# Optimization experiments

Measured on AMD Instinct MI355X. Metric: run time of the kernel, lower is better.

## Reference

```python
import jax, jax.numpy as jnp
import numpy as np

N_VOX = 500_000
C = 128
HID = 4 * C
RES = 128  # voxel grid resolution
K_OFFS = 27


def _build_sparse_coords_and_neighbors(seed=0):
    rng = np.random.default_rng(seed)
    lin = rng.choice(RES ** 3, size=N_VOX, replace=False)
    z = lin // (RES * RES)
    y = (lin // RES) % RES
    x = lin % RES
    # padded grid (RES+2)^3 so boundary lookups are in-bounds
    P = RES + 2
    grid = -np.ones(P * P * P, dtype=np.int64)
    z1, y1, x1 = z + 1, y + 1, x + 1
    grid[z1 * P * P + y1 * P + x1] = np.arange(N_VOX)
    offs = np.array([[dz, dy, dx] for dz in (-1, 0, 1) for dy in (-1, 0, 1) for dx in (-1, 0, 1)], dtype=np.int64)  # [27,3]
    nz = z1[:, None] + offs[None, :, 0]
    ny = y1[:, None] + offs[None, :, 1]
    nx = x1[:, None] + offs[None, :, 2]
    nbr = grid[nz * P * P + ny * P + nx]  # [N,27], -1 if neighbor voxel inactive
    return nbr.astype(np.int32)


def setup_inputs() -> dict:
    key = jax.random.key(0)
    ks = jax.random.split(key, 8)
    nbr = _build_sparse_coords_and_neighbors()
    scale = 0.02
    return {
        "feats": jax.random.normal(ks[0], (N_VOX, C), jnp.float32),
        "neighbor_idx": jnp.asarray(nbr),
        "conv_w": jax.random.normal(ks[1], (K_OFFS, C, C), jnp.float32) * scale,
        "conv_b": jax.random.normal(ks[2], (C,), jnp.float32) * scale,
        "ln_g": jnp.ones((C,), jnp.float32),
        "ln_b": jnp.zeros((C,), jnp.float32),
        "w1": jax.random.normal(ks[3], (C, HID), jnp.float32) * scale,
        "b1": jax.random.normal(ks[4], (HID,), jnp.float32) * scale,
        "w2": jax.random.normal(ks[5], (HID, C), jnp.float32) * scale,
        "b2": jax.random.normal(ks[6], (C,), jnp.float32) * scale,
    }


def _forward(feats, neighbor_idx, conv_w, conv_b, ln_g, ln_b, w1, b1, w2, b2):
    n, c = feats.shape
    # submanifold sparse conv3d: pad a zero row for missing (-1) neighbors
    f_pad = jnp.concatenate([feats, jnp.zeros((1, c), feats.dtype)], axis=0)
    idx = jnp.where(neighbor_idx < 0, n, neighbor_idx)  # [N,27]
    h = jnp.broadcast_to(conv_b, (n, c))
    for k in range(K_OFFS):  # fixed small kernel-offset loop; per-offset gather + GEMM
        h = h + f_pad[idx[:, k]] @ conv_w[k]
    # LayerNorm32 (fp32 math), eps=1e-6, affine
    h32 = h.astype(jnp.float32)
    mu = h32.mean(-1, keepdims=True)
    var = h32.var(-1, keepdims=True)
    hn = ((h32 - mu) * jax.lax.rsqrt(var + 1e-6) * ln_g + ln_b).astype(feats.dtype)
    # MLP: Linear -> SiLU -> Linear
    m = jax.nn.silu(hn @ w1 + b1) @ w2 + b2
    # residual h + x on sparse feats
    return m + feats


def reference(feats, neighbor_idx, conv_w, conv_b, ln_g, ln_b, w1, b1, w2, b2):
    return _forward(feats, neighbor_idx, conv_w, conv_b, ln_g, ln_b, w1, b1, w2, b2)
```

## Files before the change

kernel.cpp:

```cpp
#include <hip/hip_runtime.h>
#include <stdint.h>

#define NVOX 500000
#define NPAD 500224
#define ZERO_OFF (NVOX * 128)

typedef float  f32x4  __attribute__((ext_vector_type(4)));
typedef short  short8 __attribute__((ext_vector_type(8)));

__device__ __forceinline__ short f2bf(float x){
  unsigned u = __float_as_uint(x);
  unsigned r = (u + 0x7fffu + ((u >> 16) & 1u)) >> 16;
  return (short)r;
}

__device__ __forceinline__ void gload_lds16(const void* g, void* l){
  __builtin_amdgcn_global_load_lds(
      (const __attribute__((address_space(1))) unsigned int*)(uintptr_t)g,
      (__attribute__((address_space(3))) unsigned int*)(unsigned int)(uintptr_t)l,
      16, 0, 0);
}

__global__ void cast_feats_kernel(const float* __restrict__ f, short* __restrict__ t){
  long i = ((long)blockIdx.x * 256 + threadIdx.x) * 8;
  float4 a = *(const float4*)(f + i);
  float4 b = *(const float4*)(f + i + 4);
  short8 o = { f2bf(a.x), f2bf(a.y), f2bf(a.z), f2bf(a.w),
               f2bf(b.x), f2bf(b.y), f2bf(b.z), f2bf(b.w) };
  *(short8*)(t + i) = o;
}

__global__ void prep_nbr_kernel(const int* __restrict__ nbr, int* __restrict__ nbrT){
  __shared__ int lds_n[6912];
  const int tid = threadIdx.x;
  const long base = (long)blockIdx.x * 6912;
  #pragma unroll
  for (int i = 0; i < 27; i++){
    long g = base + i*256 + tid;
    lds_n[i*256 + tid] = (g < (long)NVOX*27) ? nbr[g] : -1;
  }
  __syncthreads();
  const int row = blockIdx.x * 256 + tid;
  #pragma unroll
  for (int k = 0; k < 27; k++){
    int id = lds_n[tid*27 + k];
    nbrT[(size_t)k*NPAD + row] = (id < 0 ? NVOX : id) * 128;
  }
}

__global__ void prep_weights_kernel(const float* __restrict__ cw, const float* __restrict__ w1,
                                    const float* __restrict__ w2,
                                    short* __restrict__ cw_sw, short* __restrict__ w1_sw,
                                    short* __restrict__ w2_sw){
  int t = blockIdx.x * 256 + threadIdx.x;
  if (t < 55296){
    int k = t >> 11, rem = t & 2047;
    int nf = rem >> 8, ks = (rem >> 6) & 3, l = rem & 63;
    int g = l >> 4, c = l & 15;
    short8 o;
    #pragma unroll
    for (int j = 0; j < 8; j++){
      int kk = ks*32 + g*8 + j;
      o[j] = f2bf(cw[(k*128 + kk)*128 + nf*16 + c]);
    }
    size_t dst = (size_t)(k*2 + (ks >> 1))*8192 + (size_t)(nf*2 + (ks & 1))*512 + (size_t)l*8;
    *(short8*)(cw_sw + dst) = o;
  } else if (t < 63488){
    int u = t - 55296;
    int nf = u >> 8, ks = (u >> 6) & 3, l = u & 63;
    int g = l >> 4, c = l & 15;
    short8 o;
    #pragma unroll
    for (int j = 0; j < 8; j++){
      int kk = ks*32 + g*8 + j;
      o[j] = f2bf(w1[kk*512 + nf*16 + c]);
    }
    *(short8*)(w1_sw + (size_t)u*8) = o;
  } else {
    int u = t - 63488;
    int c32 = u >> 9, nf = (u >> 6) & 7, l = u & 63;
    int g = l >> 4, c = l & 15;
    short8 o;
    #pragma unroll
    for (int j = 0; j < 8; j++){
      int k = c32*32 + g*8 + j;
      o[j] = f2bf(w2[k*128 + nf*16 + c]);
    }
    *(short8*)(w2_sw + (size_t)u*8) = o;
  }
}

__global__ __launch_bounds__(256, 4)
void conv_ln_v4_kernel(const short* __restrict__ table, const int* __restrict__ nbrT,
                       const short* __restrict__ cw_sw,
                       const float* __restrict__ conv_b, const float* __restrict__ ln_g,
                       const float* __restrict__ ln_b, short* __restrict__ hn16){
  __shared__ __align__(16) short lds_b[2][8192];
  const int tid = threadIdx.x;
  const int lane = tid & 63, wv = tid >> 6;
  const int l15 = lane & 15, lg = lane >> 4;
  const int rowbase = blockIdx.x * 128 + wv * 32;
  const int rowi = rowbase + l15;

  f32x4 acc[2][8];
  #pragma unroll
  for (int m = 0; m < 2; m++)
    #pragma unroll
    for (int n = 0; n < 8; n++)
      acc[m][n] = f32x4{0.f, 0.f, 0.f, 0.f};

  int idx_c[2], idx_n[2];
  #pragma unroll
  for (int m = 0; m < 2; m++) idx_c[m] = nbrT[rowi + m*16];
  #pragma unroll
  for (int m = 0; m < 2; m++) idx_n[m] = nbrT[NPAD + rowi + m*16];

  {
    const char* src = (const char*)cw_sw;
    char* dst = (char*)&lds_b[0][0];
    #pragma unroll
    for (int i = 0; i < 4; i++){ int off = i*4096 + tid*16; gload_lds16(src+off, dst+off); }
  }

  for (int k = 0; k < 27; k++){
    __syncthreads();
    {
      const char* src = (const char*)cw_sw + (size_t)(k*2 + 1)*16384;
      char* dst = (char*)&lds_b[1][0];
      #pragma unroll
      for (int i = 0; i < 4; i++){ int off = i*4096 + tid*16; gload_lds16(src+off, dst+off); }
    }
    {
      short8 af0[2], af1[2];
      #pragma unroll
      for (int m = 0; m < 2; m++)
        af0[m] = *(const short8*)(table + (size_t)(unsigned)idx_c[m] + lg*8);
      #pragma unroll
      for (int m = 0; m < 2; m++)
        af1[m] = *(const short8*)(table + (size_t)(unsigned)idx_c[m] + 32 + lg*8);
      const short* b0 = &lds_b[0][0];
      #pragma unroll
      for (int n = 0; n < 8; n++){
        short8 b = *(const short8*)(b0 + ((n*2 + 0)*64 + lane)*8);
        #pragma unroll
        for (int m = 0; m < 2; m++)
          acc[m][n] = __builtin_amdgcn_mfma_f32_16x16x32_bf16(af0[m], b, acc[m][n], 0, 0, 0);
      }
      #pragma unroll
      for (int n = 0; n < 8; n++){
        short8 b = *(const short8*)(b0 + ((n*2 + 1)*64 + lane)*8);
        #pragma unroll
        for (int m = 0; m < 2; m++)
          acc[m][n] = __builtin_amdgcn_mfma_f32_16x16x32_bf16(af1[m], b, acc[m][n], 0, 0, 0);
      }
    }
    __syncthreads();
    if (k + 1 < 27){
      const char* src = (const char*)cw_sw + (size_t)(k+1)*32768;
      char* dst = (char*)&lds_b[0][0];
      #pragma unroll
      for (int i = 0; i < 4; i++){ int off = i*4096 + tid*16; gload_lds16(src+off, dst+off); }
    }
    int idx_n2[2];
    #pragma unroll
    for (int m = 0; m < 2; m++)
      idx_n2[m] = (k + 2 < 27) ? nbrT[(size_t)(k+2)*NPAD + rowi + m*16] : ZERO_OFF;
    {
      short8 af2[2], af3[2];
      #pragma unroll
      for (int m = 0; m < 2; m++)
        af2[m] = *(const short8*)(table + (size_t)(unsigned)idx_c[m] + 64 + lg*8);
      #pragma unroll
      for (int m = 0; m < 2; m++)
        af3[m] = *(const short8*)(table + (size_t)(unsigned)idx_c[m] + 96 + lg*8);
      const short* b1 = &lds_b[1][0];
      #pragma unroll
      for (int n = 0; n < 8; n++){
        short8 b = *(const short8*)(b1 + ((n*2 + 0)*64 + lane)*8);
        #pragma unroll
        for (int m = 0; m < 2; m++)
          acc[m][n] = __builtin_amdgcn_mfma_f32_16x16x32_bf16(af2[m], b, acc[m][n], 0, 0, 0);
      }
      #pragma unroll
      for (int n = 0; n < 8; n++){
        short8 b = *(const short8*)(b1 + ((n*2 + 1)*64 + lane)*8);
        #pragma unroll
        for (int m = 0; m < 2; m++)
          acc[m][n] = __builtin_amdgcn_mfma_f32_16x16x32_bf16(af3[m], b, acc[m][n], 0, 0, 0);
      }
    }
    #pragma unroll
    for (int m = 0; m < 2; m++){ idx_c[m] = idx_n[m]; idx_n[m] = idx_n2[m]; }
  }

  float cb[8], g8[8], be[8];
  #pragma unroll
  for (int n = 0; n < 8; n++){
    cb[n] = conv_b[n*16 + l15];
    g8[n] = ln_g[n*16 + l15];
    be[n] = ln_b[n*16 + l15];
  }
  #pragma unroll
  for (int m = 0; m < 2; m++){
    #pragma unroll
    for (int r = 0; r < 4; r++){
      float s = 0.f, s2 = 0.f;
      #pragma unroll
      for (int n = 0; n < 8; n++){
        float h = acc[m][n][r] + cb[n];
        acc[m][n][r] = h;
        s += h; s2 += h*h;
      }
      #pragma unroll
      for (int msk = 1; msk < 16; msk <<= 1){
        s  += __shfl_xor(s,  msk);
        s2 += __shfl_xor(s2, msk);
      }
      float mu  = s  * 0.0078125f;
      float var = s2 * 0.0078125f - mu*mu;
      float rs  = rsqrtf(var + 1e-6f);
      int row = rowbase + m*16 + lg*4 + r;
      if (row < NVOX){
        #pragma unroll
        for (int n = 0; n < 8; n++){
          float hv = (acc[m][n][r] - mu) * rs * g8[n] + be[n];
          hn16[(size_t)row*128 + n*16 + l15] = f2bf(hv);
        }
      }
    }
  }
}

template<bool TBL>
__global__ __launch_bounds__(256, 2)
void conv_ln_kernel(const short* __restrict__ table, const float* __restrict__ feats,
                    const int* __restrict__ nbr, const short* __restrict__ cw_sw,
                    const float* __restrict__ conv_b, const float* __restrict__ ln_g,
                    const float* __restrict__ ln_b, short* __restrict__ hn16){
  __shared__ __align__(16) short lds_b[2][16384];
  const int tid = threadIdx.x;
  const int lane = tid & 63, wv = tid >> 6;
  const int l15 = lane & 15, lg = lane >> 4;
  const int rowbase = blockIdx.x * 256 + wv * 64;

  f32x4 acc[4][8];
  #pragma unroll
  for (int m = 0; m < 4; m++)
    #pragma unroll
    for (int n = 0; n < 8; n++)
      acc[m][n] = f32x4{0.f, 0.f, 0.f, 0.f};

  {
    const char* src = (const char*)cw_sw;
    char* dst = (char*)&lds_b[0][0];
    #pragma unroll
    for (int i = 0; i < 8; i++){ int off = i*4096 + tid*16; gload_lds16(src+off, dst+off); }
  }

  for (int k = 0; k < 27; k++){
    const int buf = k & 1;
    __syncthreads();
    if (k + 1 < 27){
      const char* src = (const char*)cw_sw + (size_t)(k+1)*32768;
      char* dst = (char*)&lds_b[buf ^ 1][0];
      #pragma unroll
      for (int i = 0; i < 8; i++){ int off = i*4096 + tid*16; gload_lds16(src+off, dst+off); }
    }
    int idxr[4];
    #pragma unroll
    for (int m = 0; m < 4; m++){
      int row = rowbase + m*16 + l15;
      row = row < NVOX ? row : NVOX - 1;
      int id = nbr[row*27 + k];
      idxr[m] = TBL ? (id < 0 ? NVOX : id) : id;
    }
    const short* bbase = &lds_b[buf][0];
    #pragma unroll
    for (int ks = 0; ks < 4; ks++){
      short8 af[4];
      #pragma unroll
      for (int m = 0; m < 4; m++){
        if constexpr (TBL){
          af[m] = *(const short8*)(table + (size_t)idxr[m]*128 + ks*32 + lg*8);
        } else {
          if (idxr[m] < 0){
            af[m] = short8{0,0,0,0,0,0,0,0};
          } else {
            const float* p = feats + (size_t)idxr[m]*128 + ks*32 + lg*8;
            float4 x = *(const float4*)p;
            float4 y = *(const float4*)(p + 4);
            af[m] = short8{ f2bf(x.x), f2bf(x.y), f2bf(x.z), f2bf(x.w),
                            f2bf(y.x), f2bf(y.y), f2bf(y.z), f2bf(y.w) };
          }
        }
      }
      #pragma unroll
      for (int n = 0; n < 8; n++){
        short8 b = *(const short8*)(bbase + (ks >> 1)*8192 + (((n*2 + (ks & 1))*64) + lane)*8);
        #pragma unroll
        for (int m = 0; m < 4; m++)
          acc[m][n] = __builtin_amdgcn_mfma_f32_16x16x32_bf16(af[m], b, acc[m][n], 0, 0, 0);
      }
    }
  }

  float cb[8], g8[8], be[8];
  #pragma unroll
  for (int n = 0; n < 8; n++){
    cb[n] = conv_b[n*16 + l15];
    g8[n] = ln_g[n*16 + l15];
    be[n] = ln_b[n*16 + l15];
  }
  #pragma unroll
  for (int m = 0; m < 4; m++){
    #pragma unroll
    for (int r = 0; r < 4; r++){
      float s = 0.f, s2 = 0.f;
      #pragma unroll
      for (int n = 0; n < 8; n++){
        float h = acc[m][n][r] + cb[n];
        acc[m][n][r] = h;
        s += h; s2 += h*h;
      }
      #pragma unroll
      for (int msk = 1; msk < 16; msk <<= 1){
        s  += __shfl_xor(s,  msk);
        s2 += __shfl_xor(s2, msk);
      }
      float mu  = s  * 0.0078125f;
      float var = s2 * 0.0078125f - mu*mu;
      float rs  = rsqrtf(var + 1e-6f);
      int row = rowbase + m*16 + lg*4 + r;
      if (row < NVOX){
        #pragma unroll
        for (int n = 0; n < 8; n++){
          float hv = (acc[m][n][r] - mu) * rs * g8[n] + be[n];
          hn16[(size_t)row*128 + n*16 + l15] = f2bf(hv);
        }
      }
    }
  }
}

__global__ __launch_bounds__(256, 4)
void mlp_kernel(const short* __restrict__ hn16, const float* __restrict__ feats,
                const short* __restrict__ w1_sw, const short* __restrict__ w2_sw,
                const float* __restrict__ b1, const float* __restrict__ b2,
                float* __restrict__ out){
  __shared__ __align__(16) short lds_w[2][8192];
  __shared__ __align__(16) short lds_act[4*1024];
  const int tid = threadIdx.x;
  const int lane = tid & 63, wv = tid >> 6;
  const int l15 = lane & 15, lg = lane >> 4;
  const int rowbase = blockIdx.x * 128 + wv * 32;
  short* actw = &lds_act[wv * 1024];

  f32x4 acc2[2][8];
  #pragma unroll
  for (int m = 0; m < 2; m++)
    #pragma unroll
    for (int n = 0; n < 8; n++)
      acc2[m][n] = f32x4{0.f, 0.f, 0.f, 0.f};

  int rowg[2];
  #pragma unroll
  for (int m = 0; m < 2; m++){
    int row = rowbase + m*16 + l15;
    rowg[m] = row < NVOX ? row : NVOX - 1;
  }

  short8 a1[4][2];
  #pragma unroll
  for (int ks = 0; ks < 4; ks++)
    #pragma unroll
    for (int m = 0; m < 2; m++)
      a1[ks][m] = *(const short8*)(hn16 + (size_t)rowg[m]*128 + ks*32 + lg*8);

  {
    const char* s1 = (const char*)w1_sw;
    const char* s2 = (const char*)w2_sw;
    char* dst = (char*)&lds_w[0][0];
    #pragma unroll
    for (int i = 0; i < 2; i++){ int off = i*4096 + tid*16; gload_lds16(s1+off, dst+off); }
    #pragma unroll
    for (int i = 0; i < 2; i++){ int off = i*4096 + tid*16; gload_lds16(s2+off, dst+8192+off); }
  }

  for (int ch = 0; ch < 16; ch++){
    const int buf = ch & 1;
    __syncthreads();
    if (ch + 1 < 16){
      const char* s1 = (const char*)w1_sw + (size_t)(ch+1)*8192;
      const char* s2 = (const char*)w2_sw + (size_t)(ch+1)*8192;
      char* dst = (char*)&lds_w[buf ^ 1][0];
      #pragma unroll
      for (int i = 0; i < 2; i++){ int off = i*4096 + tid*16; gload_lds16(s1+off, dst+off); }
      #pragma unroll
      for (int i = 0; i < 2; i++){ int off = i*4096 + tid*16; gload_lds16(s2+off, dst+8192+off); }
    }
    const short* w1c = &lds_w[buf][0];
    const short* w2c = &lds_w[buf][4096];

    #pragma unroll
    for (int nf = 0; nf < 2; nf++){
      f32x4 p0 = f32x4{0.f,0.f,0.f,0.f};
      f32x4 p1 = f32x4{0.f,0.f,0.f,0.f};
      #pragma unroll
      for (int ks = 0; ks < 4; ks++){
        short8 b = *(const short8*)(w1c + ((nf*4 + ks)*64 + lane)*8);
        p0 = __builtin_amdgcn_mfma_f32_16x16x32_bf16(a1[ks][0], b, p0, 0, 0, 0);
        p1 = __builtin_amdgcn_mfma_f32_16x16x32_bf16(a1[ks][1], b, p1, 0, 0, 0);
      }
      float bb1 = b1[ch*32 + nf*16 + l15];
      #pragma unroll
      for (int r = 0; r < 4; r++){
        float x0 = p0[r] + bb1;
        float x1 = p1[r] + bb1;
        float s0 = x0 / (1.f + __expf(-x0));
        float s1 = x1 / (1.f + __expf(-x1));
        int r0 = lg*4 + r;
        int r1 = 16 + lg*4 + r;
        actw[(r0*32 + nf*16 + l15) ^ ((r0 & 7) << 3)] = f2bf(s0);
        actw[(r1*32 + nf*16 + l15) ^ ((r1 & 7) << 3)] = f2bf(s1);
      }
    }

    {
      short8 a2[2];
      #pragma unroll
      for (int m = 0; m < 2; m++){
        int rowloc = m*16 + l15;
        a2[m] = *(const short8*)(actw + ((rowloc*32 + lg*8) ^ ((rowloc & 7) << 3)));
      }
      #pragma unroll
      for (int n = 0; n < 8; n++){
        short8 b = *(const short8*)(w2c + (n*64 + lane)*8);
        #pragma unroll
        for (int m = 0; m < 2; m++)
          acc2[m][n] = __builtin_amdgcn_mfma_f32_16x16x32_bf16(a2[m], b, acc2[m][n], 0, 0, 0);
      }
    }
  }

  float bb2[8];
  #pragma unroll
  for (int n = 0; n < 8; n++) bb2[n] = b2[n*16 + l15];
  #pragma unroll
  for (int m = 0; m < 2; m++)
    #pragma unroll
    for (int n = 0; n < 8; n++)
      #pragma unroll
      for (int r = 0; r < 4; r++){
        int row = rowbase + m*16 + lg*4 + r;
        if (row < NVOX){
          size_t ci = (size_t)row*128 + n*16 + l15;
          out[ci] = acc2[m][n][r] + bb2[n] + feats[ci];
        }
      }
}

extern "C" void kernel_launch(void* const* d_in, const int* in_sizes, int n_in,
                              void* d_out, int out_size, void* d_ws, size_t ws_size,
                              hipStream_t stream){
  const float* feats = (const float*)d_in[0];
  const int*   nbr   = (const int*)  d_in[1];
  const float* cw    = (const float*)d_in[2];
  const float* cb    = (const float*)d_in[3];
  const float* lng   = (const float*)d_in[4];
  const float* lnb   = (const float*)d_in[5];
  const float* w1    = (const float*)d_in[6];
  const float* b1    = (const float*)d_in[7];
  const float* w2    = (const float*)d_in[8];
  const float* b2    = (const float*)d_in[9];
  float* out = (float*)d_out;

  char* ws = (char*)d_ws;
  const size_t TABLE_B = (size_t)(NVOX + 1) * 256;
  const size_t HN_B    = (size_t)NVOX * 256;
  const size_t CW_B    = 55296u * 16u;
  const size_t W1_B    = 8192u * 16u;
  const size_t W2_B    = 8192u * 16u;
  const size_t NBRT_B  = (size_t)27 * NPAD * 4;
  const size_t need_full = TABLE_B + HN_B + CW_B + W1_B + W2_B;
  const size_t need_pf   = need_full + NBRT_B;

  if (ws_size >= need_pf){
    short* table = (short*)ws;
    short* hn16  = (short*)(ws + TABLE_B);
    short* cw_sw = (short*)(ws + TABLE_B + HN_B);
    short* w1_sw = (short*)(ws + TABLE_B + HN_B + CW_B);
    short* w2_sw = (short*)(ws + TABLE_B + HN_B + CW_B + W1_B);
    int*   nbrT  = (int*)  (ws + need_full);

    cast_feats_kernel<<<31250, 256, 0, stream>>>(feats, table);
    hipMemsetAsync((void*)(table + (size_t)NVOX * 128), 0, 256, stream);
    prep_nbr_kernel<<<1954, 256, 0, stream>>>(nbr, nbrT);
    prep_weights_kernel<<<280, 256, 0, stream>>>(cw, w1, w2, cw_sw, w1_sw, w2_sw);
    conv_ln_v4_kernel<<<3907, 256, 0, stream>>>(table, nbrT, cw_sw, cb, lng, lnb, hn16);
    mlp_kernel<<<3907, 256, 0, stream>>>(hn16, feats, w1_sw, w2_sw, b1, b2, out);
  } else if (ws_size >= need_full){
    short* table = (short*)ws;
    short* hn16  = (short*)(ws + TABLE_B);
    short* cw_sw = (short*)(ws + TABLE_B + HN_B);
    short* w1_sw = (short*)(ws + TABLE_B + HN_B + CW_B);
    short* w2_sw = (short*)(ws + TABLE_B + HN_B + CW_B + W1_B);

    cast_feats_kernel<<<31250, 256, 0, stream>>>(feats, table);
    hipMemsetAsync((void*)(table + (size_t)NVOX * 128), 0, 256, stream);
    prep_weights_kernel<<<280, 256, 0, stream>>>(cw, w1, w2, cw_sw, w1_sw, w2_sw);
    conv_ln_kernel<true><<<1954, 256, 0, stream>>>(table, feats, nbr, cw_sw, cb, lng, lnb, hn16);
    mlp_kernel<<<3907, 256, 0, stream>>>(hn16, feats, w1_sw, w2_sw, b1, b2, out);
  } else {
    short* hn16  = (short*)ws;
    short* cw_sw = (short*)(ws + HN_B);
    short* w1_sw = (short*)(ws + HN_B + CW_B);
    short* w2_sw = (short*)(ws + HN_B + CW_B + W1_B);

    prep_weights_kernel<<<280, 256, 0, stream>>>(cw, w1, w2, cw_sw, w1_sw, w2_sw);
    conv_ln_kernel<false><<<1954, 256, 0, stream>>>(nullptr, feats, nbr, cw_sw, cb, lng, lnb, hn16);
    mlp_kernel<<<3907, 256, 0, stream>>>(hn16, feats, w1_sw, w2_sw, b1, b2, out);
  }
}
```

Before: 939.8 us.

## Keep MLP hidden activations in registers via transposed MFMA and lane shuffles

The first MLP GEMM now computes its transposed product by swapping the MFMA operands. Each lane therefore holds 4 consecutive hidden columns, which lets the bias come in as one float4 and the SiLU outputs be packed with v_cvt_pk_bf16. The per-wave LDS staging buffer for activations is removed and replaced by cross-lane shuffles that build the A operand of the second GEMM directly in registers. This is meant to cut LDS write/read traffic and barriers in the MLP. It costs extra shuffle instructions and more register pressure, and launch bounds drop from 4 to 3 blocks per SIMD to match.

Measured after the change: 864.2 us. 1.09x faster.

```diff
diff --git a/kernel.cpp b/kernel.cpp
--- a/kernel.cpp
+++ b/kernel.cpp
@@ -12,6 +12,12 @@
   unsigned u = __float_as_uint(x);
   unsigned r = (u + 0x7fffu + ((u >> 16) & 1u)) >> 16;
   return (short)r;
+}
+
+__device__ __forceinline__ int cvt_pk_bf16(float lo, float hi){
+  int r;
+  asm("v_cvt_pk_bf16_f32 %0, %1, %2" : "=v"(r) : "v"(lo), "v"(hi));
+  return r;
 }
 
 __device__ __forceinline__ void gload_lds16(const void* g, void* l){
@@ -342,18 +348,19 @@
   }
 }
 
-__global__ __launch_bounds__(256, 4)
+__global__ __launch_bounds__(256, 3)
 void mlp_kernel(const short* __restrict__ hn16, const float* __restrict__ feats,
                 const short* __restrict__ w1_sw, const short* __restrict__ w2_sw,
                 const float* __restrict__ b1, const float* __restrict__ b2,
                 float* __restrict__ out){
   __shared__ __align__(16) short lds_w[2][8192];
-  __shared__ __align__(16) short lds_act[4*1024];
   const int tid = threadIdx.x;
   const int lane = tid & 63, wv = tid >> 6;
   const int l15 = lane & 15, lg = lane >> 4;
   const int rowbase = blockIdx.x * 128 + wv * 32;
-  short* actw = &lds_act[wv * 1024];
+  const int sl0 = l15 + 32*(lg & 1);
+  const int sl1 = sl0 + 16;
+  const bool hiHalf = (lg >> 1) != 0;
 
   f32x4 acc2[2][8];
   #pragma unroll
@@ -401,44 +408,54 @@
     const short* w1c = &lds_w[buf][0];
     const short* w2c = &lds_w[buf][4096];
 
-    #pragma unroll
-    for (int nf = 0; nf < 2; nf++){
-      f32x4 p0 = f32x4{0.f,0.f,0.f,0.f};
-      f32x4 p1 = f32x4{0.f,0.f,0.f,0.f};
-      #pragma unroll
-      for (int ks = 0; ks < 4; ks++){
-        short8 b = *(const short8*)(w1c + ((nf*4 + ks)*64 + lane)*8);
-        p0 = __builtin_amdgcn_mfma_f32_16x16x32_bf16(a1[ks][0], b, p0, 0, 0, 0);
-        p1 = __builtin_amdgcn_mfma_f32_16x16x32_bf16(a1[ks][1], b, p1, 0, 0, 0);
-      }
-      float bb1 = b1[ch*32 + nf*16 + l15];
-      #pragma unroll
-      for (int r = 0; r < 4; r++){
-        float x0 = p0[r] + bb1;
-        float x1 = p1[r] + bb1;
-        float s0 = x0 / (1.f + __expf(-x0));
-        float s1 = x1 / (1.f + __expf(-x1));
-        int r0 = lg*4 + r;
-        int r1 = 16 + lg*4 + r;
-        actw[(r0*32 + nf*16 + l15) ^ ((r0 & 7) << 3)] = f2bf(s0);
-        actw[(r1*32 + nf*16 + l15) ^ ((r1 & 7) << 3)] = f2bf(s1);
-      }
-    }
-
+    float4 b1v0 = *(const float4*)(b1 + ch*32 +  0 + lg*4);
+    float4 b1v1 = *(const float4*)(b1 + ch*32 + 16 + lg*4);
+
+    f32x4 p00 = f32x4{0.f,0.f,0.f,0.f}, p01 = f32x4{0.f,0.f,0.f,0.f};
+    f32x4 p10 = f32x4{0.f,0.f,0.f,0.f}, p11 = f32x4{0.f,0.f,0.f,0.f};
+    #pragma unroll
+    for (int ks = 0; ks < 4; ks++){
+      short8 wA0 = *(const short8*)(w1c + ((0*4 + ks)*64 + lane)*8);
+      short8 wA1 = *(const short8*)(w1c + ((1*4 + ks)*64 + lane)*8);
+      p00 = __builtin_amdgcn_mfma_f32_16x16x32_bf16(wA0, a1[ks][0], p00, 0, 0, 0);
+      p01 = __builtin_amdgcn_mfma_f32_16x16x32_bf16(wA0, a1[ks][1], p01, 0, 0, 0);
+      p10 = __builtin_amdgcn_mfma_f32_16x16x32_bf16(wA1, a1[ks][0], p10, 0, 0, 0);
+      p11 = __builtin_amdgcn_mfma_f32_16x16x32_bf16(wA1, a1[ks][1], p11, 0, 0, 0);
+    }
+
+    int pk00[2], pk01[2], pk10[2], pk11[2];
     {
-      short8 a2[2];
-      #pragma unroll
-      for (int m = 0; m < 2; m++){
-        int rowloc = m*16 + l15;
-        a2[m] = *(const short8*)(actw + ((rowloc*32 + lg*8) ^ ((rowloc & 7) << 3)));
-      }
-      #pragma unroll
-      for (int n = 0; n < 8; n++){
-        short8 b = *(const short8*)(w2c + (n*64 + lane)*8);
-        #pragma unroll
-        for (int m = 0; m < 2; m++)
-          acc2[m][n] = __builtin_amdgcn_mfma_f32_16x16x32_bf16(a2[m], b, acc2[m][n], 0, 0, 0);
-      }
+      float s0, s1v, s2v, s3;
+      #define SILU4(P, BV, PK)                                            \
+        s0 = (P)[0] + (BV).x; s0 = s0 / (1.f + __expf(-s0));              \
+        s1v = (P)[1] + (BV).y; s1v = s1v / (1.f + __expf(-s1v));          \
+        s2v = (P)[2] + (BV).z; s2v = s2v / (1.f + __expf(-s2v));          \
+        s3 = (P)[3] + (BV).w; s3 = s3 / (1.f + __expf(-s3));              \
+        (PK)[0] = cvt_pk_bf16(s0, s1v); (PK)[1] = cvt_pk_bf16(s2v, s3);
+      SILU4(p00, b1v0, pk00)
+      SILU4(p01, b1v0, pk01)
+      SILU4(p10, b1v1, pk10)
+      SILU4(p11, b1v1, pk11)
+      #undef SILU4
+    }
+
+    union { int i[4]; short8 s; } a2u0, a2u1;
+    #pragma unroll
+    for (int w = 0; w < 4; w++){
+      int src = (w < 2) ? sl0 : sl1;
+      int t0 = __shfl(pk00[w & 1], src);
+      int t1 = __shfl(pk10[w & 1], src);
+      a2u0.i[w] = hiHalf ? t1 : t0;
+      int u0 = __shfl(pk01[w & 1], src);
+      int u1 = __shfl(pk11[w & 1], src);
+      a2u1.i[w] = hiHalf ? u1 : u0;
+    }
+
+    #pragma unroll
+    for (int n = 0; n < 8; n++){
+      short8 b = *(const short8*)(w2c + (n*64 + lane)*8);
+      acc2[0][n] = __builtin_amdgcn_mfma_f32_16x16x32_bf16(a2u0.s, b, acc2[0][n], 0, 0, 0);
+      acc2[1][n] = __builtin_amdgcn_mfma_f32_16x16x32_bf16(a2u1.s, b, acc2[1][n], 0, 0, 0);
     }
   }
 
```
